# Kernel optimization log

Measured on AMD Instinct MI355X. Metric: run time of the kernel, lower is better.

The kernel has to match this reference:

```python
import jax, jax.numpy as jnp
import numpy as np

EPS = 1e-5          # InstanceNorm eps (torch default)
KERNEL = 25         # moving_avg_kernel_size
TAU = 1.0           # gumbel softmax temperature
REGIME_NUM = 8


def _inorm(x):
    # InstanceNorm1d without affine on (N, C, L): normalize over last dim (biased var)
    m = x.mean(-1, keepdims=True)
    v = ((x - m) ** 2).mean(-1, keepdims=True)
    return (x - m) * jax.lax.rsqrt(v + EPS)


def _lbr(x, W, b):
    # Linear -> InstanceNorm (over last dim) -> exact GELU
    return jax.nn.gelu(_inorm(x @ W + b), approximate=False)


def _moving_avg(x, k):
    # x: (B, L, C); edge-replicate pad (k-1)//2 on both sides, sliding mean via cumsum
    p = (k - 1) // 2
    xp = jnp.concatenate([jnp.repeat(x[:, :1], p, axis=1), x,
                          jnp.repeat(x[:, -1:], p, axis=1)], axis=1)
    cs = jnp.concatenate([jnp.zeros_like(xp[:, :1]), jnp.cumsum(xp, axis=1)], axis=1)
    return (cs[:, k:] - cs[:, :-k]) / k  # (B, L, C)


def _encode(x, Ws, bs, Wt, bt):
    # inputs - inputs[:, 0:1]; series decomposition; seasonal+trend branches
    x = x - x[:, :1]
    mm = _moving_avg(x, KERNEL)
    return _lbr(x - mm, Ws, bs) + _lbr(mm, Wt, bt)  # (B, L, H)


def reference(inputs_longterm, inputs_shortterm,
              Ws, bs, Wt, bt,
              Wh1, bh1, Wl1, bl1, Wh2, bh2, Wl2, bl2, Wh3, bh3, Wl3, bl3,
              Wr, br, proto):
    e_lt = _encode(inputs_longterm, Ws, bs, Wt, bt)   # (B, L_lt, H)
    e_st = _encode(inputs_shortterm, Ws, bs, Wt, bt)  # (B, L_st, H)

    # RegimeEncoder: alternate hidden-dim and lookback-dim LinearBatchRelu layers
    o = _lbr(e_lt, Wh1, bh1)
    o = jnp.swapaxes(_lbr(jnp.swapaxes(o, 1, 2), Wl1, bl1), 1, 2)
    o = _lbr(o, Wh2, bh2)
    o = jnp.swapaxes(_lbr(jnp.swapaxes(o, 1, 2), Wl2, bl2), 1, 2)
    o = _lbr(o, Wh3, bh3)
    o = jnp.swapaxes(_lbr(jnp.swapaxes(o, 1, 2), Wl3, bl3), 1, 2)  # (B, L_lt//8, H)
    logits = o.reshape(o.shape[0], -1) @ Wr + br  # (B, R)

    # gumbel_softmax(hard=True) with straight-through estimator
    g = jax.random.gumbel(jax.random.key(42), logits.shape, logits.dtype)
    y_soft = jax.nn.softmax((logits + g) / TAU, axis=-1)
    y_hard = jax.nn.one_hot(jnp.argmax(y_soft, axis=-1), REGIME_NUM, dtype=logits.dtype)
    w = y_hard - jax.lax.stop_gradient(y_soft) + y_soft  # (B, R)

    # weighted sum over regime prototypes, then combine with encoded shortterm
    sel = jnp.einsum('br,rnhmo->bnhmo', w, proto)          # (B, L_st, H, M, 3)
    out = jnp.einsum('bnh,bnhmo->bmo', e_st, sel)          # (B, M, 3)
    B = out.shape[0]
    return jax.nn.softmax(out.reshape(B, -1), axis=-1).reshape(out.shape)


def setup_inputs() -> dict:
    key = jax.random.key(0)
    ks = jax.random.split(key, 24)
    B, L_lt, L_st, C, H, R, M = 32, 512, 128, 9, 128, 8, 64
    s = 0.02
    d = {
        'inputs_longterm':  jax.random.normal(ks[0], (B, L_lt, C), jnp.float32),
        'inputs_shortterm': jax.random.normal(ks[1], (B, L_st, C), jnp.float32),
        'Ws': jax.random.normal(ks[2], (C, H), jnp.float32) * s,
        'bs': jnp.zeros((H,), jnp.float32),
        'Wt': jax.random.normal(ks[3], (C, H), jnp.float32) * s,
        'bt': jnp.zeros((H,), jnp.float32),
        'Wh1': jax.random.normal(ks[4], (H, H), jnp.float32) * s,
        'bh1': jnp.zeros((H,), jnp.float32),
        'Wl1': jax.random.normal(ks[5], (L_lt, L_lt // 2), jnp.float32) * s,
        'bl1': jnp.zeros((L_lt // 2,), jnp.float32),
        'Wh2': jax.random.normal(ks[6], (H, H), jnp.float32) * s,
        'bh2': jnp.zeros((H,), jnp.float32),
        'Wl2': jax.random.normal(ks[7], (L_lt // 2, L_lt // 4), jnp.float32) * s,
        'bl2': jnp.zeros((L_lt // 4,), jnp.float32),
        'Wh3': jax.random.normal(ks[8], (H, H), jnp.float32) * s,
        'bh3': jnp.zeros((H,), jnp.float32),
        'Wl3': jax.random.normal(ks[9], (L_lt // 4, L_lt // 8), jnp.float32) * s,
        'bl3': jnp.zeros((L_lt // 8,), jnp.float32),
        'Wr': jax.random.normal(ks[10], (H * L_lt // 8, R), jnp.float32) * s,
        'br': jnp.zeros((R,), jnp.float32),
        'proto': jax.random.normal(ks[11], (R, L_st, H, M, 3), jnp.float32),
    }
    return d
```

## Files before the change

### kernel.cpp

```cpp
#include <hip/hip_runtime.h>
#include <math.h>

#define EPS 1e-5f

__device__ __forceinline__ float gelu_exact(float x) {
    return 0.5f * x * (1.0f + erff(x * 0.7071067811865476f));
}

__device__ float block_sum(float v, float* red) {
    int lane = threadIdx.x & 63, wid = threadIdx.x >> 6;
#pragma unroll
    for (int off = 32; off > 0; off >>= 1) v += __shfl_down(v, off, 64);
    if (lane == 0) red[wid] = v;
    __syncthreads();
    int nw = ((int)blockDim.x + 63) >> 6;
    float s = red[0];
    for (int w = 1; w < nw; w++) s += red[w];
    __syncthreads();
    return s;
}

__device__ float block_max(float v, float* red) {
    int lane = threadIdx.x & 63, wid = threadIdx.x >> 6;
#pragma unroll
    for (int off = 32; off > 0; off >>= 1) v = fmaxf(v, __shfl_down(v, off, 64));
    if (lane == 0) red[wid] = v;
    __syncthreads();
    int nw = ((int)blockDim.x + 63) >> 6;
    float s = red[0];
    for (int w = 1; w < nw; w++) s = fmaxf(s, red[w]);
    __syncthreads();
    return s;
}

__device__ void threefry2x32(unsigned k0, unsigned k1, unsigned x0, unsigned x1,
                             unsigned& o0, unsigned& o1) {
    unsigned ks[3] = {k0, k1, k0 ^ k1 ^ 0x1BD11BDAu};
    const unsigned rot[2][4] = {{13u, 15u, 26u, 6u}, {17u, 29u, 16u, 24u}};
    x0 += ks[0]; x1 += ks[1];
#pragma unroll
    for (int i = 0; i < 5; i++) {
#pragma unroll
        for (int j = 0; j < 4; j++) {
            unsigned r = rot[i & 1][j];
            x0 += x1;
            x1 = (x1 << r) | (x1 >> (32 - r));
            x1 ^= x0;
        }
        x0 += ks[(i + 1) % 3];
        x1 += ks[(i + 2) % 3] + (unsigned)(i + 1);
    }
    o0 = x0; o1 = x1;
}

__device__ float gumbel_at(int j) {
    unsigned o0, o1;
    threefry2x32(0u, 42u, 0u, (unsigned)j, o0, o1);
    unsigned bits = o0 ^ o1;
    float f = __uint_as_float((bits >> 9) | 0x3F800000u) - 1.0f;
    float u = fmaxf(f + 1.17549435e-38f, 1.17549435e-38f);
    return -logf(-logf(u));
}

__global__ __launch_bounds__(256) void encode_st_kernel(
    const float* __restrict__ x_st,
    const float* __restrict__ Ws, const float* __restrict__ bs,
    const float* __restrict__ Wt, const float* __restrict__ bt,
    float* __restrict__ e_st) {
    const int b = blockIdx.y;
    const int w = threadIdx.x >> 6, ln = threadIdx.x & 63;
    const int L = 128;
    const int l = blockIdx.x * 4 + w;
    __shared__ float xw_all[4][228];
    __shared__ float sm_all[4][20];
    float* xw = xw_all[w];
    float* sm = sm_all[w];
    const float* xb = x_st + (size_t)b * L * 9;
#pragma unroll
    for (int q = 0; q < 4; q++) {
        int f = ln + 64 * q;
        if (f < 225) {
            int row = f / 9, c = f - row * 9;
            int rr = l - 12 + row;
            rr = rr < 0 ? 0 : (rr >= L ? L - 1 : rr);
            xw[f] = xb[(size_t)rr * 9 + c];
        }
    }
    __syncthreads();
    if (ln < 9) {
        float s = 0.f;
#pragma unroll
        for (int j = 0; j < 25; j++) s += xw[j * 9 + ln];
        float x0 = xb[ln];
        float mm = (s - 25.f * x0) * (1.0f / 25.0f);
        sm[ln] = (xw[108 + ln] - x0) - mm;
        sm[ln + 10] = mm;
    }
    __syncthreads();
    float ysA = bs[ln], ysB = bs[ln + 64];
    float ytA = bt[ln], ytB = bt[ln + 64];
#pragma unroll
    for (int c = 0; c < 9; c++) {
        float sv = sm[c], mv = sm[c + 10];
        ysA += sv * Ws[c * 128 + ln];
        ysB += sv * Ws[c * 128 + ln + 64];
        ytA += mv * Wt[c * 128 + ln];
        ytB += mv * Wt[c * 128 + ln + 64];
    }
    float sa = ysA + ysB, sb2 = ytA + ytB;
#pragma unroll
    for (int off = 32; off > 0; off >>= 1) {
        sa += __shfl_xor(sa, off, 64);
        sb2 += __shfl_xor(sb2, off, 64);
    }
    float ms = sa * (1.0f / 128.0f), mt = sb2 * (1.0f / 128.0f);
    float dA = ysA - ms, dB = ysB - ms;
    float tA = ytA - mt, tB = ytB - mt;
    float qa = dA * dA + dB * dB, qb = tA * tA + tB * tB;
#pragma unroll
    for (int off = 32; off > 0; off >>= 1) {
        qa += __shfl_xor(qa, off, 64);
        qb += __shfl_xor(qb, off, 64);
    }
    float inva = rsqrtf(qa * (1.0f / 128.0f) + EPS);
    float invb = rsqrtf(qb * (1.0f / 128.0f) + EPS);
    float* eo = e_st + ((size_t)b * L + l) * 128;
    eo[ln] = gelu_exact(dA * inva) + gelu_exact(tA * invb);
    eo[ln + 64] = gelu_exact(dB * inva) + gelu_exact(tB * invb);
}

__global__ __launch_bounds__(256) void enc_h1(
    const float* __restrict__ x_lt,
    const float* __restrict__ Ws, const float* __restrict__ bs,
    const float* __restrict__ Wt, const float* __restrict__ bt,
    const float* __restrict__ Wh1, const float* __restrict__ bh1,
    float* __restrict__ O1T) {
    constexpr int K = 128, N = 128, WR = 2, KC = 64;
    constexpr int CG = N / 4;
    constexpr int SG = 64 / CG;
    constexpr int RW = SG * WR;
    constexpr int MT = 16;
    constexpr int WSZ = KC * N;
    __shared__ __align__(16) float lds[WSZ + MT * K];
    __shared__ float xwin[40 * 9];
    __shared__ float x0s[9];
    __shared__ float smS[16 * 9], smT[16 * 9];
    const int t = threadIdx.x;
    const int w = t >> 6, ln = t & 63;
    const int bx = blockIdx.x;
    const int b = bx >> 5;
    const int l0 = (bx & 31) * 16;
    const float* xb = x_lt + (size_t)b * 512 * 9;
    for (int f = t; f < 360; f += 256) {
        int row = f / 9, c = f - row * 9;
        int rr = l0 - 12 + row;
        rr = rr < 0 ? 0 : (rr > 511 ? 511 : rr);
        xwin[f] = xb[(size_t)rr * 9 + c];
    }
    if (t < 9) x0s[t] = xb[t];
    __syncthreads();
    if (t < 144) {
        int li = t / 9, c = t - (t / 9) * 9;
        float s = 0.f;
#pragma unroll
        for (int j = 0; j < 25; j++) s += xwin[(li + j) * 9 + c];
        float x0 = x0s[c];
        float mm = (s - 25.f * x0) * (1.0f / 25.0f);
        smS[t] = (xwin[(li + 12) * 9 + c] - x0) - mm;
        smT[t] = mm;
    }
    __syncthreads();
    float* As = lds + WSZ;
    for (int q = 0; q < 4; q++) {
        int li = w * 4 + q;
        const float* sS = smS + li * 9;
        const float* sT = smT + li * 9;
        float ysA = bs[ln], ysB = bs[ln + 64];
        float ytA = bt[ln], ytB = bt[ln + 64];
#pragma unroll
        for (int c = 0; c < 9; c++) {
            float sv = sS[c], mv = sT[c];
            ysA += sv * Ws[c * 128 + ln];
            ysB += sv * Ws[c * 128 + ln + 64];
            ytA += mv * Wt[c * 128 + ln];
            ytB += mv * Wt[c * 128 + ln + 64];
        }
        float sa = ysA + ysB, sb2 = ytA + ytB;
#pragma unroll
        for (int off = 32; off > 0; off >>= 1) {
            sa += __shfl_xor(sa, off, 64);
            sb2 += __shfl_xor(sb2, off, 64);
        }
        float ms = sa * (1.0f / 128.0f), mt = sb2 * (1.0f / 128.0f);
        float dA = ysA - ms, dB = ysB - ms;
        float tA = ytA - mt, tB = ytB - mt;
        float qa = dA * dA + dB * dB, qb = tA * tA + tB * tB;
#pragma unroll
        for (int off = 32; off > 0; off >>= 1) {
            qa += __shfl_xor(qa, off, 64);
            qb += __shfl_xor(qb, off, 64);
        }
        float inva = rsqrtf(qa * (1.0f / 128.0f) + EPS);
        float invb = rsqrtf(qb * (1.0f / 128.0f) + EPS);
        As[li * 128 + ln] = gelu_exact(dA * inva) + gelu_exact(tA * invb);
        As[li * 128 + ln + 64] = gelu_exact(dB * inva) + gelu_exact(tB * invb);
    }
    __syncthreads();
    const int sg = ln / CG;
    const int n0 = (ln % CG) * 4;
    float4 acc[WR];
    {
        float4 bv = *(const float4*)(bh1 + n0);
#pragma unroll
        for (int j = 0; j < WR; j++) acc[j] = bv;
    }
    const float* ap = As + (w * RW + sg * WR) * K;
    for (int kc0 = 0; kc0 < K; kc0 += KC) {
        if (kc0) __syncthreads();
        {
            const float4* wg = (const float4*)(Wh1 + (size_t)kc0 * N);
            float4* wl4 = (float4*)lds;
#pragma unroll
            for (int i = 0; i < WSZ / 4 / 256; i++)
                wl4[t + i * 256] = wg[t + i * 256];
        }
        __syncthreads();
#pragma unroll 2
        for (int k = 0; k < KC; k += 4) {
            const float* wp = lds + k * N + n0;
            float4 w0 = *(const float4*)(wp);
            float4 w1 = *(const float4*)(wp + N);
            float4 w2 = *(const float4*)(wp + 2 * N);
            float4 w3 = *(const float4*)(wp + 3 * N);
#pragma unroll
            for (int j = 0; j < WR; j++) {
                float4 a4 = *(const float4*)(ap + j * K + kc0 + k);
                acc[j].x += a4.x * w0.x; acc[j].y += a4.x * w0.y;
                acc[j].z += a4.x * w0.z; acc[j].w += a4.x * w0.w;
                acc[j].x += a4.y * w1.x; acc[j].y += a4.y * w1.y;
                acc[j].z += a4.y * w1.z; acc[j].w += a4.y * w1.w;
                acc[j].x += a4.z * w2.x; acc[j].y += a4.z * w2.y;
                acc[j].z += a4.z * w2.z; acc[j].w += a4.z * w2.w;
                acc[j].x += a4.w * w3.x; acc[j].y += a4.w * w3.y;
                acc[j].z += a4.w * w3.z; acc[j].w += a4.w * w3.w;
            }
        }
    }
    float4 res[WR];
#pragma unroll
    for (int j = 0; j < WR; j++) {
        float s = acc[j].x + acc[j].y + acc[j].z + acc[j].w;
#pragma unroll
        for (int off = CG / 2; off > 0; off >>= 1) s += __shfl_xor(s, off, 64);
        float m = s * (1.0f / (float)N);
        float dx = acc[j].x - m, dy = acc[j].y - m, dz = acc[j].z - m, dw = acc[j].w - m;
        float q = dx * dx + dy * dy + dz * dz + dw * dw;
#pragma unroll
        for (int off = CG / 2; off > 0; off >>= 1) q += __shfl_xor(q, off, 64);
        float inv = rsqrtf(q * (1.0f / (float)N) + EPS);
        res[j].x = gelu_exact(dx * inv);
        res[j].y = gelu_exact(dy * inv);
        res[j].z = gelu_exact(dz * inv);
        res[j].w = gelu_exact(dw * inv);
    }
    __syncthreads();
#pragma unroll
    for (int j = 0; j < WR; j++) {
        int rl = w * RW + sg * WR + j;
        *(float4*)(lds + rl * (N + 4) + n0) = res[j];
    }
    __syncthreads();
    float* ob = O1T + (size_t)bx * 16;
    for (int e = t; e < MT * N; e += 256) {
        int r = e & 15, n = e >> 4;
        ob[(size_t)n * 16384 + r] = lds[r * (N + 4) + n];
    }
}

template <int K, int N, int WR, int KC, bool TRANS>
__global__ __launch_bounds__(256) void lbr_wave(
    const float* __restrict__ A, int S, int ABOFF,
    const float* __restrict__ W, const float* __restrict__ bias,
    float* __restrict__ out, int OROWS, int OBOFF) {
    constexpr int CG = N / 4;
    constexpr int SG = 64 / CG;
    constexpr int RW = SG * WR;
    constexpr int MT = 4 * RW;
    constexpr int LOG2MT = (MT == 8) ? 3 : ((MT == 16) ? 4 : 5);
    constexpr int WSZ = KC * N;
    constexpr int ASZ = 4 * RW * K;
    static_assert(WSZ >= MT * (N + 4), "TRANS tile must fit in W region");
    static_assert((WSZ / 4) % 256 == 0, "W chunk loads must be exact");
    __shared__ __align__(16) float lds[WSZ + ASZ];
    const int t = threadIdx.x;
    const int w = t >> 6, ln = t & 63;
    const int sg = ln / CG;
    const int n0 = (ln % CG) * 4;
    const int b = blockIdx.y;
    const int r0b = blockIdx.x * MT;
    const int r0w = r0b + w * RW;
    float* Wl = lds;
    float* As = lds + WSZ + w * RW * K;
    const float* Ab = A + (size_t)b * ABOFF;
    for (int idx = ln; idx < RW * (K / 4); idx += 64) {
        int rr = idx / (K / 4), kk = idx % (K / 4);
        float4 v = *(const float4*)(Ab + (size_t)(r0w + rr) * S + kk * 4);
        *(float4*)(As + rr * K + kk * 4) = v;
    }
    float4 acc[WR];
    {
        float4 bv = *(const float4*)(bias + n0);
#pragma unroll
        for (int j = 0; j < WR; j++) acc[j] = bv;
    }
    const float* ap = As + (sg * WR) * K;
    for (int kc0 = 0; kc0 < K; kc0 += KC) {
        __syncthreads();
        {
            const float4* wg = (const float4*)(W + (size_t)kc0 * N);
            float4* wl4 = (float4*)Wl;
#pragma unroll
            for (int i = 0; i < WSZ / 4 / 256; i++)
                wl4[t + i * 256] = wg[t + i * 256];
        }
        __syncthreads();
#pragma unroll 2
        for (int k = 0; k < KC; k += 4) {
            const float* wp = Wl + k * N + n0;
            float4 w0 = *(const float4*)(wp);
            float4 w1 = *(const float4*)(wp + N);
            float4 w2 = *(const float4*)(wp + 2 * N);
            float4 w3 = *(const float4*)(wp + 3 * N);
#pragma unroll
            for (int j = 0; j < WR; j++) {
                float4 a4 = *(const float4*)(ap + j * K + kc0 + k);
                acc[j].x += a4.x * w0.x; acc[j].y += a4.x * w0.y;
                acc[j].z += a4.x * w0.z; acc[j].w += a4.x * w0.w;
                acc[j].x += a4.y * w1.x; acc[j].y += a4.y * w1.y;
                acc[j].z += a4.y * w1.z; acc[j].w += a4.y * w1.w;
                acc[j].x += a4.z * w2.x; acc[j].y += a4.z * w2.y;
                acc[j].z += a4.z * w2.z; acc[j].w += a4.z * w2.w;
                acc[j].x += a4.w * w3.x; acc[j].y += a4.w * w3.y;
                acc[j].z += a4.w * w3.z; acc[j].w += a4.w * w3.w;
            }
        }
    }
    float4 res[WR];
#pragma unroll
    for (int j = 0; j < WR; j++) {
        float s = acc[j].x + acc[j].y + acc[j].z + acc[j].w;
#pragma unroll
        for (int off = CG / 2; off > 0; off >>= 1) s += __shfl_xor(s, off, 64);
        float m = s * (1.0f / (float)N);
        float dx = acc[j].x - m, dy = acc[j].y - m, dz = acc[j].z - m, dw = acc[j].w - m;
        float q = dx * dx + dy * dy + dz * dz + dw * dw;
#pragma unroll
        for (int off = CG / 2; off > 0; off >>= 1) q += __shfl_xor(q, off, 64);
        float inv = rsqrtf(q * (1.0f / (float)N) + EPS);
        res[j].x = gelu_exact(dx * inv);
        res[j].y = gelu_exact(dy * inv);
        res[j].z = gelu_exact(dz * inv);
        res[j].w = gelu_exact(dw * inv);
    }
    if constexpr (TRANS) {
        __syncthreads();
#pragma unroll
        for (int j = 0; j < WR; j++) {
            int rl = w * RW + sg * WR + j;
            *(float4*)(lds + rl * (N + 4) + n0) = res[j];
        }
        __syncthreads();
        float* ob = out + (size_t)b * OBOFF + r0b;
        for (int e = t; e < MT * N; e += 256) {
            int r = e & (MT - 1), n = e >> LOG2MT;
            ob[(size_t)n * OROWS + r] = lds[r * (N + 4) + n];
        }
    } else {
        float* ob = out + (size_t)b * OBOFF;
#pragma unroll
        for (int j = 0; j < WR; j++) {
            int row = r0w + sg * WR + j;
            *(float4*)(ob + (size_t)row * N + n0) = res[j];
        }
    }
}

__global__ __launch_bounds__(256) void l3_logits(
    const float* __restrict__ O5T, const float* __restrict__ Wl3,
    const float* __restrict__ bl3, const float* __restrict__ Wr,
    const float* __restrict__ br, float* __restrict__ sel_w, int* __restrict__ sel_r) {
    constexpr int N = 64, K = 128;
    constexpr int CG = 16, WR = 8, RW = 32;
    __shared__ __align__(16) float Wl[K * N];
    __shared__ __align__(16) float As[128 * K];
    __shared__ float redl[4][8];
    const int t = threadIdx.x, w = t >> 6, ln = t & 63;
    const int b = blockIdx.x;
#pragma unroll
    for (int i = 0; i < 16; i++) {
        int idx = t + i * 256;
        int rr = idx >> 5, kk = idx & 31;
        *(float4*)(&As[rr * 128 + kk * 4]) =
            *(const float4*)(O5T + (size_t)rr * 4096 + b * 128 + kk * 4);
    }
    {
        const float4* wg = (const float4*)(Wl3);
        float4* wl4 = (float4*)Wl;
#pragma unroll
        for (int i = 0; i < 8; i++) wl4[t + i * 256] = wg[t + i * 256];
    }
    __syncthreads();
    const int sg = ln / CG;
    const int n0 = (ln % CG) * 4;
    const int row0 = w * RW + sg * WR;
    float4 acc[WR];
    {
        float4 bv = *(const float4*)(bl3 + n0);
#pragma unroll
        for (int j = 0; j < WR; j++) acc[j] = bv;
    }
#pragma unroll 2
    for (int k = 0; k < K; k += 4) {
        const float* wp = Wl + k * N + n0;
        float4 w0 = *(const float4*)(wp);
        float4 w1 = *(const float4*)(wp + N);
        float4 w2 = *(const float4*)(wp + 2 * N);
        float4 w3 = *(const float4*)(wp + 3 * N);
#pragma unroll
        for (int j = 0; j < WR; j++) {
            float4 a4 = *(const float4*)(&As[(row0 + j) * 128 + k]);
            acc[j].x += a4.x * w0.x; acc[j].y += a4.x * w0.y;
            acc[j].z += a4.x * w0.z; acc[j].w += a4.x * w0.w;
            acc[j].x += a4.y * w1.x; acc[j].y += a4.y * w1.y;
            acc[j].z += a4.y * w1.z; acc[j].w += a4.y * w1.w;
            acc[j].x += a4.z * w2.x; acc[j].y += a4.z * w2.y;
            acc[j].z += a4.z * w2.z; acc[j].w += a4.z * w2.w;
            acc[j].x += a4.w * w3.x; acc[j].y += a4.w * w3.y;
            acc[j].z += a4.w * w3.z; acc[j].w += a4.w * w3.w;
        }
    }
    float4 res[WR];
#pragma unroll
    for (int j = 0; j < WR; j++) {
        float s = acc[j].x + acc[j].y + acc[j].z + acc[j].w;
#pragma unroll
        for (int off = CG / 2; off > 0; off >>= 1) s += __shfl_xor(s, off, 64);
        float m = s * (1.0f / (float)N);
        float dx = acc[j].x - m, dy = acc[j].y - m, dz = acc[j].z - m, dw = acc[j].w - m;
        float q = dx * dx + dy * dy + dz * dz + dw * dw;
#pragma unroll
        for (int off = CG / 2; off > 0; off >>= 1) q += __shfl_xor(q, off, 64);
        float inv = rsqrtf(q * (1.0f / (float)N) + EPS);
        res[j].x = gelu_exact(dx * inv);
        res[j].y = gelu_exact(dy * inv);
        res[j].z = gelu_exact(dz * inv);
        res[j].w = gelu_exact(dw * inv);
    }
    __syncthreads();
#pragma unroll
    for (int j = 0; j < WR; j++) {
        int row = row0 + j;
        *(float4*)(&As[row * 68 + n0]) = res[j];
    }
    __syncthreads();
    float acl[8] = {0, 0, 0, 0, 0, 0, 0, 0};
#pragma unroll 4
    for (int q = 0; q < 32; q++) {
        int i = q * 256 + t;
        int l4 = i >> 7, h = i & 127;
        float v = As[h * 68 + l4];
        const float4* wr = (const float4*)(Wr + (size_t)i * 8);
        float4 w0 = wr[0], w1 = wr[1];
        acl[0] += v * w0.x; acl[1] += v * w0.y; acl[2] += v * w0.z; acl[3] += v * w0.w;
        acl[4] += v * w1.x; acl[5] += v * w1.y; acl[6] += v * w1.z; acl[7] += v * w1.w;
    }
#pragma unroll
    for (int j = 0; j < 8; j++)
#pragma unroll
        for (int off = 32; off > 0; off >>= 1) acl[j] += __shfl_xor(acl[j], off, 64);
    if (ln == 0)
        for (int j = 0; j < 8; j++) redl[w][j] = acl[j];
    __syncthreads();
    if (t == 0) {
        float z[8];
        for (int j = 0; j < 8; j++) {
            float lg = br[j] + redl[0][j] + redl[1][j] + redl[2][j] + redl[3][j];
            z[j] = lg + gumbel_at(b * 8 + j);
        }
        int am = 0;
        float zm = z[0];
        for (int j = 1; j < 8; j++)
            if (z[j] > zm) { zm = z[j]; am = j; }
        float ssum = 0.f;
        for (int j = 0; j < 8; j++) ssum += expf(z[j] - zm);
        float s = 1.0f / ssum;
        sel_w[b] = (1.0f - s) + s;
        sel_r[b] = am;
    }
}

__global__ __launch_bounds__(192, 4) void einsum_nsplit(
    const float* __restrict__ e_st, const float* __restrict__ proto,
    const int* __restrict__ sel_r, float* __restrict__ part) {
    const int n = blockIdx.x, r = blockIdx.y, hz = blockIdx.z, t = threadIdx.x;
    const int w = t >> 6, ln = t & 63;
    const int rg = ln >> 4;
    const int q4 = (w * 16 + (ln & 15)) * 4;
    __shared__ int loc[32];
    __shared__ int s_gs;
    if (t == 0) {
        int g = 0;
        for (int bb = 0; bb < 32; bb++)
            if (sel_r[bb] == r) loc[g++] = bb;
        s_gs = g;
    }
    __syncthreads();
    const int gs = s_gs;
    if (gs == 0) return;
    __shared__ __align__(16) float es[64][12];
    const float* pb = proto + (((size_t)r * 128 + n) * 128 + hz * 64) * 192;
    float* po = part + (size_t)hz * (32 * 128 * 192);
    for (int s0 = 0; s0 < gs; s0 += 8) {
        int np = gs - s0 < 8 ? gs - s0 : 8;
        __syncthreads();
        for (int i = t; i < 512; i += 192) {
            int sb = i >> 6, h = i & 63;
            float v = 0.f;
            if (sb < np)
                v = e_st[((size_t)loc[s0 + sb] * 128 + n) * 128 + hz * 64 + h];
            es[h][sb] = v;
        }
        __syncthreads();
        float4 a[8];
#pragma unroll
        for (int sb = 0; sb < 8; sb++) a[sb] = make_float4(0.f, 0.f, 0.f, 0.f);
#pragma unroll 4
        for (int hh = 0; hh < 16; hh++) {
            int row = hh * 4 + rg;
            float4 pv = *(const float4*)(pb + (size_t)row * 192 + q4);
            float4 e0 = *(const float4*)(&es[row][0]);
            float4 e1 = *(const float4*)(&es[row][4]);
#define ACC4(j, s) a[j].x += (s) * pv.x; a[j].y += (s) * pv.y; \
                   a[j].z += (s) * pv.z; a[j].w += (s) * pv.w;
            ACC4(0, e0.x) ACC4(1, e0.y) ACC4(2, e0.z) ACC4(3, e0.w)
            ACC4(4, e1.x) ACC4(5, e1.y) ACC4(6, e1.z) ACC4(7, e1.w)
#undef ACC4
        }
#pragma unroll
        for (int sb = 0; sb < 8; sb++) {
            a[sb].x += __shfl_xor(a[sb].x, 16, 64);
            a[sb].y += __shfl_xor(a[sb].y, 16, 64);
            a[sb].z += __shfl_xor(a[sb].z, 16, 64);
            a[sb].w += __shfl_xor(a[sb].w, 16, 64);
            a[sb].x += __shfl_xor(a[sb].x, 32, 64);
            a[sb].y += __shfl_xor(a[sb].y, 32, 64);
            a[sb].z += __shfl_xor(a[sb].z, 32, 64);
            a[sb].w += __shfl_xor(a[sb].w, 32, 64);
        }
        if (ln < 16) {
#pragma unroll
            for (int sb = 0; sb < 8; sb++) {
                if (sb < np) {
                    int bb = loc[s0 + sb];
                    *(float4*)(po + ((size_t)bb * 128 + n) * 192 + q4) = a[sb];
                }
            }
        }
    }
}

__global__ void finalize_kernel(const float* __restrict__ part, const float* __restrict__ sel_w,
                                float* __restrict__ out) {
    int b = blockIdx.x, t = threadIdx.x;
    __shared__ float red[4];
    const float* p0 = part + (size_t)b * 128 * 192 + t;
    const float* p1 = p0 + (size_t)32 * 128 * 192;
    float v = 0.f;
#pragma unroll 8
    for (int c = 0; c < 128; c++) {
        v += p0[(size_t)c * 192];
        v += p1[(size_t)c * 192];
    }
    v *= sel_w[b];
    float mx = block_max(v, red);
    float e = expf(v - mx);
    float s = block_sum(e, red);
    out[(size_t)b * 192 + t] = e / s;
}

extern "C" void kernel_launch(void* const* d_in, const int* in_sizes, int n_in,
                              void* d_out, int out_size, void* d_ws, size_t ws_size,
                              hipStream_t stream) {
    const float* in_lt = (const float*)d_in[0];
    const float* in_st = (const float*)d_in[1];
    const float* Ws  = (const float*)d_in[2];  const float* bs  = (const float*)d_in[3];
    const float* Wt  = (const float*)d_in[4];  const float* bt  = (const float*)d_in[5];
    const float* Wh1 = (const float*)d_in[6];  const float* bh1 = (const float*)d_in[7];
    const float* Wl1 = (const float*)d_in[8];  const float* bl1 = (const float*)d_in[9];
    const float* Wh2 = (const float*)d_in[10]; const float* bh2 = (const float*)d_in[11];
    const float* Wl2 = (const float*)d_in[12]; const float* bl2 = (const float*)d_in[13];
    const float* Wh3 = (const float*)d_in[14]; const float* bh3 = (const float*)d_in[15];
    const float* Wl3 = (const float*)d_in[16]; const float* bl3 = (const float*)d_in[17];
    const float* Wr  = (const float*)d_in[18]; const float* br  = (const float*)d_in[19];
    const float* proto = (const float*)d_in[20];
    float* out = (float*)d_out;

    float* ws = (float*)d_ws;
    size_t off = 0;
    float* e_lt = ws + off; off += (size_t)32 * 512 * 128;
    float* e_st = ws + off; off += (size_t)32 * 128 * 128;
    float* O1T = ws + off; off += (size_t)128 * 16384;
    float* O2T = ws + off; off += (size_t)256 * 4096;
    float* O3T = ws + off; off += (size_t)128 * 8192;
    float* O4T = ws + off; off += (size_t)128 * 4096;
    float* O5T = ws + off; off += (size_t)128 * 4096;
    float* O6 = ws + off; off += (size_t)32 * 128 * 64;
    float* part = ws + off; off += (size_t)2 * 32 * 128 * 192;
    float* sel_w = ws + off; off += 32;
    int* sel_r = (int*)(ws + off); off += 32;
    (void)e_lt; (void)O6;

    encode_st_kernel<<<dim3(32, 32), 256, 0, stream>>>(in_st, Ws, bs, Wt, bt, e_st);
    enc_h1<<<dim3(1024), 256, 0, stream>>>(in_lt, Ws, bs, Wt, bt, Wh1, bh1, O1T);
    lbr_wave<512, 256, 2, 32, true><<<dim3(16, 32), 256, 0, stream>>>(
        O1T, 16384, 512, Wl1, bl1, O2T, 4096, 128);
    lbr_wave<128, 128, 2, 64, true><<<dim3(16, 32), 256, 0, stream>>>(
        O2T, 4096, 128, Wh2, bh2, O3T, 8192, 256);
    lbr_wave<256, 128, 1, 64, true><<<dim3(16, 32), 256, 0, stream>>>(
        O3T, 8192, 256, Wl2, bl2, O4T, 4096, 128);
    lbr_wave<128, 128, 1, 64, true><<<dim3(16, 32), 256, 0, stream>>>(
        O4T, 4096, 128, Wh3, bh3, O5T, 4096, 128);
    l3_logits<<<32, 256, 0, stream>>>(O5T, Wl3, bl3, Wr, br, sel_w, sel_r);
    einsum_nsplit<<<dim3(128, 8, 2), 192, 0, stream>>>(e_st, proto, sel_r, part);
    finalize_kernel<<<32, 192, 0, stream>>>(part, sel_w, out);
}
```

Baseline: 331.5 us.

## Fuse short-term encode into enc_h1 and add double-buffered L1 lookback kernel

Folds the short-term series encoder into the enc_h1 launch by giving it 256 extra blocks that write e_st and exit early, removing one kernel launch. It also replaces the generic lbr_wave instance for the first lookback layer with a dedicated kernel. That kernel uses more rows per wave, half as many blocks, and double-buffered weight chunks with a register prefetch, so global loads overlap the FMA loop. The cost is a larger LDS footprint (about 96KB), which lowers occupancy, and fewer blocks in flight for the 512x256 GEMM.

```diff
diff --git a/kernel.cpp b/kernel.cpp
--- a/kernel.cpp
+++ b/kernel.cpp
@@ -62,79 +62,12 @@
     return -logf(-logf(u));
 }
 
-__global__ __launch_bounds__(256) void encode_st_kernel(
-    const float* __restrict__ x_st,
-    const float* __restrict__ Ws, const float* __restrict__ bs,
-    const float* __restrict__ Wt, const float* __restrict__ bt,
-    float* __restrict__ e_st) {
-    const int b = blockIdx.y;
-    const int w = threadIdx.x >> 6, ln = threadIdx.x & 63;
-    const int L = 128;
-    const int l = blockIdx.x * 4 + w;
-    __shared__ float xw_all[4][228];
-    __shared__ float sm_all[4][20];
-    float* xw = xw_all[w];
-    float* sm = sm_all[w];
-    const float* xb = x_st + (size_t)b * L * 9;
-#pragma unroll
-    for (int q = 0; q < 4; q++) {
-        int f = ln + 64 * q;
-        if (f < 225) {
-            int row = f / 9, c = f - row * 9;
-            int rr = l - 12 + row;
-            rr = rr < 0 ? 0 : (rr >= L ? L - 1 : rr);
-            xw[f] = xb[(size_t)rr * 9 + c];
-        }
-    }
-    __syncthreads();
-    if (ln < 9) {
-        float s = 0.f;
-#pragma unroll
-        for (int j = 0; j < 25; j++) s += xw[j * 9 + ln];
-        float x0 = xb[ln];
-        float mm = (s - 25.f * x0) * (1.0f / 25.0f);
-        sm[ln] = (xw[108 + ln] - x0) - mm;
-        sm[ln + 10] = mm;
-    }
-    __syncthreads();
-    float ysA = bs[ln], ysB = bs[ln + 64];
-    float ytA = bt[ln], ytB = bt[ln + 64];
-#pragma unroll
-    for (int c = 0; c < 9; c++) {
-        float sv = sm[c], mv = sm[c + 10];
-        ysA += sv * Ws[c * 128 + ln];
-        ysB += sv * Ws[c * 128 + ln + 64];
-        ytA += mv * Wt[c * 128 + ln];
-        ytB += mv * Wt[c * 128 + ln + 64];
-    }
-    float sa = ysA + ysB, sb2 = ytA + ytB;
-#pragma unroll
-    for (int off = 32; off > 0; off >>= 1) {
-        sa += __shfl_xor(sa, off, 64);
-        sb2 += __shfl_xor(sb2, off, 64);
-    }
-    float ms = sa * (1.0f / 128.0f), mt = sb2 * (1.0f / 128.0f);
-    float dA = ysA - ms, dB = ysB - ms;
-    float tA = ytA - mt, tB = ytB - mt;
-    float qa = dA * dA + dB * dB, qb = tA * tA + tB * tB;
-#pragma unroll
-    for (int off = 32; off > 0; off >>= 1) {
-        qa += __shfl_xor(qa, off, 64);
-        qb += __shfl_xor(qb, off, 64);
-    }
-    float inva = rsqrtf(qa * (1.0f / 128.0f) + EPS);
-    float invb = rsqrtf(qb * (1.0f / 128.0f) + EPS);
-    float* eo = e_st + ((size_t)b * L + l) * 128;
-    eo[ln] = gelu_exact(dA * inva) + gelu_exact(tA * invb);
-    eo[ln + 64] = gelu_exact(dB * inva) + gelu_exact(tB * invb);
-}
-
 __global__ __launch_bounds__(256) void enc_h1(
-    const float* __restrict__ x_lt,
+    const float* __restrict__ x_lt, const float* __restrict__ x_st,
     const float* __restrict__ Ws, const float* __restrict__ bs,
     const float* __restrict__ Wt, const float* __restrict__ bt,
     const float* __restrict__ Wh1, const float* __restrict__ bh1,
-    float* __restrict__ O1T) {
+    float* __restrict__ O1T, float* __restrict__ e_st) {
     constexpr int K = 128, N = 128, WR = 2, KC = 64;
     constexpr int CG = N / 4;
     constexpr int SG = 64 / CG;
@@ -148,13 +81,21 @@
     const int t = threadIdx.x;
     const int w = t >> 6, ln = t & 63;
     const int bx = blockIdx.x;
-    const int b = bx >> 5;
-    const int l0 = (bx & 31) * 16;
-    const float* xb = x_lt + (size_t)b * 512 * 9;
+    const bool st = bx >= 1024;
+    int b, l0, L;
+    const float* xb;
+    if (st) {
+        int ub = bx - 1024;
+        b = ub >> 3; l0 = (ub & 7) * 16; L = 128;
+        xb = x_st + (size_t)b * 128 * 9;
+    } else {
+        b = bx >> 5; l0 = (bx & 31) * 16; L = 512;
+        xb = x_lt + (size_t)b * 512 * 9;
+    }
     for (int f = t; f < 360; f += 256) {
         int row = f / 9, c = f - row * 9;
         int rr = l0 - 12 + row;
-        rr = rr < 0 ? 0 : (rr > 511 ? 511 : rr);
+        rr = rr < 0 ? 0 : (rr > L - 1 ? L - 1 : rr);
         xwin[f] = xb[(size_t)rr * 9 + c];
     }
     if (t < 9) x0s[t] = xb[t];
@@ -202,9 +143,18 @@
         }
         float inva = rsqrtf(qa * (1.0f / 128.0f) + EPS);
         float invb = rsqrtf(qb * (1.0f / 128.0f) + EPS);
-        As[li * 128 + ln] = gelu_exact(dA * inva) + gelu_exact(tA * invb);
-        As[li * 128 + ln + 64] = gelu_exact(dB * inva) + gelu_exact(tB * invb);
-    }
+        float vA = gelu_exact(dA * inva) + gelu_exact(tA * invb);
+        float vB = gelu_exact(dB * inva) + gelu_exact(tB * invb);
+        if (st) {
+            float* eo = e_st + ((size_t)b * 128 + (l0 + li)) * 128;
+            eo[ln] = vA;
+            eo[ln + 64] = vB;
+        } else {
+            As[li * 128 + ln] = vA;
+            As[li * 128 + ln + 64] = vB;
+        }
+    }
+    if (st) return;
     __syncthreads();
     const int sg = ln / CG;
     const int n0 = (ln % CG) * 4;
@@ -274,6 +224,107 @@
     for (int e = t; e < MT * N; e += 256) {
         int r = e & 15, n = e >> 4;
         ob[(size_t)n * 16384 + r] = lds[r * (N + 4) + n];
+    }
+}
+
+__global__ __launch_bounds__(256) void lbr_l1(
+    const float* __restrict__ A, const float* __restrict__ W,
+    const float* __restrict__ bias, float* __restrict__ out) {
+    constexpr int K = 512, N = 256, WR = 4, KC = 32;
+    constexpr int RW = WR, MT = 4 * RW;
+    constexpr int WSZ = KC * N;
+    constexpr int NCH = K / KC;
+    __shared__ __align__(16) float lds[2 * WSZ + 4 * RW * K];
+    const int t = threadIdx.x, w = t >> 6, ln = t & 63;
+    const int n0 = ln * 4;
+    const int b = blockIdx.y;
+    const int r0b = blockIdx.x * MT;
+    const int r0w = r0b + w * RW;
+    float* As = lds + 2 * WSZ + w * RW * K;
+    const float* Ab = A + (size_t)b * 512;
+    for (int idx = ln; idx < RW * (K / 4); idx += 64) {
+        int rr = idx >> 7, kk = idx & 127;
+        *(float4*)(As + rr * K + kk * 4) =
+            *(const float4*)(Ab + (size_t)(r0w + rr) * 16384 + kk * 4);
+    }
+    const float4* Wg4 = (const float4*)W;
+    float4 pf[8];
+#pragma unroll
+    for (int i = 0; i < 8; i++) pf[i] = Wg4[t + i * 256];
+    {
+        float4* wb4 = (float4*)lds;
+#pragma unroll
+        for (int i = 0; i < 8; i++) wb4[t + i * 256] = pf[i];
+    }
+    float4 acc[WR];
+    {
+        float4 bv = *(const float4*)(bias + n0);
+#pragma unroll
+        for (int j = 0; j < WR; j++) acc[j] = bv;
+    }
+    __syncthreads();
+    for (int c = 0; c < NCH; c++) {
+        if (c + 1 < NCH) {
+#pragma unroll
+            for (int i = 0; i < 8; i++)
+                pf[i] = Wg4[(c + 1) * (WSZ / 4) + t + i * 256];
+        }
+        const float* Wb = lds + (c & 1) * WSZ;
+        const int kc0 = c * KC;
+#pragma unroll
+        for (int k = 0; k < KC; k += 4) {
+            const float* wp = Wb + k * N + n0;
+            float4 w0 = *(const float4*)(wp);
+            float4 w1 = *(const float4*)(wp + N);
+            float4 w2 = *(const float4*)(wp + 2 * N);
+            float4 w3 = *(const float4*)(wp + 3 * N);
+#pragma unroll
+            for (int j = 0; j < WR; j++) {
+                float4 a4 = *(const float4*)(As + j * K + kc0 + k);
+                acc[j].x += a4.x * w0.x; acc[j].y += a4.x * w0.y;
+                acc[j].z += a4.x * w0.z; acc[j].w += a4.x * w0.w;
+                acc[j].x += a4.y * w1.x; acc[j].y += a4.y * w1.y;
+                acc[j].z += a4.y * w1.z; acc[j].w += a4.y * w1.w;
+                acc[j].x += a4.z * w2.x; acc[j].y += a4.z * w2.y;
+                acc[j].z += a4.z * w2.z; acc[j].w += a4.z * w2.w;
+                acc[j].x += a4.w * w3.x; acc[j].y += a4.w * w3.y;
+                acc[j].z += a4.w * w3.z; acc[j].w += a4.w * w3.w;
+            }
+        }
+        if (c + 1 < NCH) {
+            float4* wb4 = (float4*)(lds + ((c + 1) & 1) * WSZ);
+#pragma unroll
+            for (int i = 0; i < 8; i++) wb4[t + i * 256] = pf[i];
+        }
+        __syncthreads();
+    }
+    float4 res[WR];
+#pragma unroll
+    for (int j = 0; j < WR; j++) {
+        float s = acc[j].x + acc[j].y + acc[j].z + acc[j].w;
+#pragma unroll
+        for (int off = 32; off > 0; off >>= 1) s += __shfl_xor(s, off, 64);
+        float m = s * (1.0f / (float)N);
+        float dx = acc[j].x - m, dy = acc[j].y - m, dz = acc[j].z - m, dw = acc[j].w - m;
+        float q = dx * dx + dy * dy + dz * dz + dw * dw;
+#pragma unroll
+        for (int off = 32; off > 0; off >>= 1) q += __shfl_xor(q, off, 64);
+        float inv = rsqrtf(q * (1.0f / (float)N) + EPS);
+        res[j].x = gelu_exact(dx * inv);
+        res[j].y = gelu_exact(dy * inv);
+        res[j].z = gelu_exact(dz * inv);
+        res[j].w = gelu_exact(dw * inv);
+    }
+#pragma unroll
+    for (int j = 0; j < WR; j++) {
+        int rl = w * RW + j;
+        *(float4*)(lds + rl * (N + 4) + n0) = res[j];
+    }
+    __syncthreads();
+    float* ob = out + (size_t)b * 128 + r0b;
+    for (int e = t; e < MT * N; e += 256) {
+        int r = e & 15, n = e >> 4;
+        ob[(size_t)n * 4096 + r] = lds[r * (N + 4) + n];
     }
 }
 
@@ -620,10 +671,8 @@
     int* sel_r = (int*)(ws + off); off += 32;
     (void)e_lt; (void)O6;
 
-    encode_st_kernel<<<dim3(32, 32), 256, 0, stream>>>(in_st, Ws, bs, Wt, bt, e_st);
-    enc_h1<<<dim3(1024), 256, 0, stream>>>(in_lt, Ws, bs, Wt, bt, Wh1, bh1, O1T);
-    lbr_wave<512, 256, 2, 32, true><<<dim3(16, 32), 256, 0, stream>>>(
-        O1T, 16384, 512, Wl1, bl1, O2T, 4096, 128);
+    enc_h1<<<dim3(1280), 256, 0, stream>>>(in_lt, in_st, Ws, bs, Wt, bt, Wh1, bh1, O1T, e_st);
+    lbr_l1<<<dim3(8, 32), 256, 0, stream>>>(O1T, Wl1, bl1, O2T);
     lbr_wave<128, 128, 2, 64, true><<<dim3(16, 32), 256, 0, stream>>>(
         O2T, 4096, 128, Wh2, bh2, O3T, 8192, 256);
     lbr_wave<256, 128, 1, 64, true><<<dim3(16, 32), 256, 0, stream>>>(
```

Result: slower. 351.5 us (+6.0%).
